# Kernel optimization log

Measured on AMD Instinct MI355X. Metric: run time of the kernel, lower is better.

The kernel has to match this reference:

```python
import jax, jax.numpy as jnp
import numpy as np

DIM = 4096
N_EXPERTS = 64
TOP_K = 2
TOKENS = 16384


def setup_inputs() -> dict:
    key = jax.random.key(0)
    k1, k2 = jax.random.split(key)
    x = jax.random.normal(k1, (TOKENS, DIM), dtype=jnp.float32)
    # nn.Linear weight is [out_features, in_features] = [n_experts, dim]
    w_gate = jax.random.normal(k2, (N_EXPERTS, DIM), dtype=jnp.float32) * (1.0 / np.sqrt(DIM))
    return {"x": x, "w_gate": w_gate}


def reference(x, w_gate):
    # logits: [tokens, n_experts]
    logits = jnp.einsum("td,ed->te", x, w_gate)
    gates = jax.nn.softmax(logits, axis=-1)
    topk_vals, topk_idx = jax.lax.top_k(gates, TOP_K)
    return (gates, topk_vals, topk_idx)
```

## Files before the change

kernel.cpp:

```cpp
#include <hip/hip_runtime.h>
#include <stdint.h>

typedef float f32x4 __attribute__((ext_vector_type(4)));
typedef _Float16 f16;
typedef _Float16 f16x8 __attribute__((ext_vector_type(8)));

#define TOKENS 16384
#define DIM    4096
#define NEXP   64
#define BM     32
#define KC     64
#define NCHUNK (DIM/KC)
#define GSZ    (TOKENS*NEXP)
#define VSZ    (TOKENS*2)
#define BUFSZ  24576
#define LSTR   68

__device__ __forceinline__ void split8(f32x4 a, f32x4 b, f16x8& h, f16x8& l) {
#pragma unroll
    for (int i = 0; i < 4; ++i) {
        float v = a[i]; f16 hi = (f16)v;
        h[i] = hi; l[i] = (f16)(v - (float)hi);
    }
#pragma unroll
    for (int i = 0; i < 4; ++i) {
        float v = b[i]; f16 hi = (f16)v;
        h[4+i] = hi; l[4+i] = (f16)(v - (float)hi);
    }
}

__global__ __launch_bounds__(256, 2)
void router_kernel(const float* __restrict__ x,
                   const float* __restrict__ w,
                   float* __restrict__ out)
{
    __shared__ unsigned char smem[2*BUFSZ];

    const int tid  = threadIdx.x;
    const int tok0 = blockIdx.x * BM;

    const int xrow = tid >> 3, xks = tid & 7;
    const int we   = tid >> 2, wq  = tid & 3;

    const float* xg = x + (size_t)(tok0 + xrow)*DIM + xks*8;
    const float* wg = w + (size_t)we*DIM + wq*16;

    const int lane = tid & 63;
    const int wv   = tid >> 6;
    const int mt   = wv >> 1;
    const int ntb  = (wv & 1) * 2;
    const int frow = mt*16 + (lane & 15);
    const int fk   = lane >> 4;
    const int swz  = lane & 7;

    f32x4 acc[2] = {{0,0,0,0},{0,0,0,0}};

    f32x4 xr0, xr1, wr0, wr1, wr2, wr3;
    xr0 = ((const f32x4*)xg)[0];  xr1 = ((const f32x4*)xg)[1];
    wr0 = ((const f32x4*)wg)[0];  wr1 = ((const f32x4*)wg)[1];
    wr2 = ((const f32x4*)wg)[2];  wr3 = ((const f32x4*)wg)[3];

    auto cw = [&](unsigned char* base) {
        f16* XH = (f16*)base;
        f16* XL = XH + BM*KC;
        f16* WH = XL + BM*KC;
        f16* WL = WH + NEXP*KC;
        f16x8 h, l;
        split8(xr0, xr1, h, l);
        int s = xks ^ (xrow & 7);
        *(f16x8*)(XH + xrow*KC + s*8) = h;
        *(f16x8*)(XL + xrow*KC + s*8) = l;
        split8(wr0, wr1, h, l);
        s = (wq*2) ^ (we & 7);
        *(f16x8*)(WH + we*KC + s*8) = h;
        *(f16x8*)(WL + we*KC + s*8) = l;
        split8(wr2, wr3, h, l);
        s = (wq*2 + 1) ^ (we & 7);
        *(f16x8*)(WH + we*KC + s*8) = h;
        *(f16x8*)(WL + we*KC + s*8) = l;
    };

    cw(smem);

    for (int kc = 0; kc < NCHUNK; ++kc) {
        if (kc + 1 < NCHUNK) {
            const float* xp = xg + (kc+1)*KC;
            const float* wp = wg + (kc+1)*KC;
            xr0 = ((const f32x4*)xp)[0];  xr1 = ((const f32x4*)xp)[1];
            wr0 = ((const f32x4*)wp)[0];  wr1 = ((const f32x4*)wp)[1];
            wr2 = ((const f32x4*)wp)[2];  wr3 = ((const f32x4*)wp)[3];
        }
        asm volatile("s_waitcnt lgkmcnt(0)" ::: "memory");
        __builtin_amdgcn_s_barrier();

        const unsigned char* base = smem + (size_t)(kc & 1)*BUFSZ;
        const f16* XH = (const f16*)base;
        const f16* XL = XH + BM*KC;
        const f16* WH = XL + BM*KC;
        const f16* WL = WH + NEXP*KC;
#pragma unroll
        for (int ks = 0; ks < 2; ++ks) {
            const int sl = (ks*4 + fk) ^ swz;
            f16x8 ah = *(const f16x8*)(XH + frow*KC + sl*8);
            f16x8 al = *(const f16x8*)(XL + frow*KC + sl*8);
#pragma unroll
            for (int n = 0; n < 2; ++n) {
                const int e = (ntb + n)*16 + (lane & 15);
                f16x8 bh = *(const f16x8*)(WH + e*KC + sl*8);
                f16x8 bl = *(const f16x8*)(WL + e*KC + sl*8);
                acc[n] = __builtin_amdgcn_mfma_f32_16x16x32_f16(ah, bh, acc[n], 0, 0, 0);
                acc[n] = __builtin_amdgcn_mfma_f32_16x16x32_f16(ah, bl, acc[n], 0, 0, 0);
                acc[n] = __builtin_amdgcn_mfma_f32_16x16x32_f16(al, bh, acc[n], 0, 0, 0);
            }
        }
        if (kc + 1 < NCHUNK) cw(smem + (size_t)((kc+1) & 1)*BUFSZ);
    }

    float* lg = (float*)smem;
#pragma unroll
    for (int n = 0; n < 2; ++n) {
        const int e = (ntb + n)*16 + (lane & 15);
#pragma unroll
        for (int i = 0; i < 4; ++i) {
            const int trow = mt*16 + fk*4 + i;
            lg[trow*LSTR + e] = acc[n][i];
        }
    }
    __syncthreads();

    const int st = tid >> 3;
    const int sg = tid & 7;
    const float* rowp = lg + st*LSTR + sg*8;
    float g[8];
#pragma unroll
    for (int j = 0; j < 8; ++j) g[j] = rowp[j];
    float m = g[0];
#pragma unroll
    for (int j = 1; j < 8; ++j) m = fmaxf(m, g[j]);
#pragma unroll
    for (int off = 1; off < 8; off <<= 1) m = fmaxf(m, __shfl_xor(m, off));
    float s = 0.f;
#pragma unroll
    for (int j = 0; j < 8; ++j) { g[j] = expf(g[j] - m); s += g[j]; }
#pragma unroll
    for (int off = 1; off < 8; off <<= 1) s += __shfl_xor(s, off);
    const float inv = 1.0f / s;
#pragma unroll
    for (int j = 0; j < 8; ++j) g[j] *= inv;

    const size_t t = (size_t)tok0 + st;
    f32x4 g0 = {g[0],g[1],g[2],g[3]}, g1 = {g[4],g[5],g[6],g[7]};
    *(f32x4*)(out + t*NEXP + sg*8)     = g0;
    *(f32x4*)(out + t*NEXP + sg*8 + 4) = g1;

    float v1 = g[0]; int i1 = sg*8;
    float v2 = -__builtin_inff(); int i2 = 1 << 30;
#pragma unroll
    for (int j = 1; j < 8; ++j) {
        float lv = g[j]; int li = sg*8 + j;
        bool b1 = (lv > v1) || (lv == v1 && li < i1);
        bool b2 = (lv > v2) || (lv == v2 && li < i2);
        float pv1 = v1; int pi1 = i1;
        v1 = b1 ? lv : v1;  i1 = b1 ? li : i1;
        v2 = b1 ? pv1 : (b2 ? lv : v2);
        i2 = b1 ? pi1 : (b2 ? li : i2);
    }
#pragma unroll
    for (int off = 1; off < 8; off <<= 1) {
        float ov1 = __shfl_xor(v1, off); int oi1 = __shfl_xor(i1, off);
        float ov2 = __shfl_xor(v2, off); int oi2 = __shfl_xor(i2, off);
        bool afirst = (v1 > ov1) || (v1 == ov1 && i1 < oi1);
        float nv1, nv2; int ni1, ni2;
        if (afirst) {
            nv1 = v1; ni1 = i1;
            bool b = (v2 > ov1) || (v2 == ov1 && i2 < oi1);
            nv2 = b ? v2 : ov1; ni2 = b ? i2 : oi1;
        } else {
            nv1 = ov1; ni1 = oi1;
            bool b = (ov2 > v1) || (ov2 == v1 && oi2 < i1);
            nv2 = b ? ov2 : v1; ni2 = b ? oi2 : i1;
        }
        v1 = nv1; i1 = ni1; v2 = nv2; i2 = ni2;
    }
    if (sg == 0) {
        out[GSZ + 2*t]           = v1;
        out[GSZ + 2*t + 1]       = v2;
        out[GSZ + VSZ + 2*t]     = (float)i1;
        out[GSZ + VSZ + 2*t + 1] = (float)i2;
    }
}

extern "C" void kernel_launch(void* const* d_in, const int* in_sizes, int n_in,
                              void* d_out, int out_size, void* d_ws, size_t ws_size,
                              hipStream_t stream) {
    (void)in_sizes; (void)n_in; (void)d_ws; (void)ws_size; (void)out_size;
    const float* x = (const float*)d_in[0];
    const float* w = (const float*)d_in[1];
    float* out     = (float*)d_out;
    dim3 grid(TOKENS / BM);
    dim3 block(256);
    router_kernel<<<grid, block, 0, stream>>>(x, w, out);
}
```

Baseline: 380.8 us.

## Pre-split gate weights into fp16 fragments and split-K across eight waves

A small pre-pass kernel splits the fp32 gate weights into hi/lo fp16 halves, stored in MFMA fragment order in the workspace. The main kernel then reads x and weight fragments straight from global memory into registers, with no LDS staging or per-chunk barriers. Each of the eight waves in a 512-thread block handles a K slice for all 32 tokens and 64 experts, and the partial sums are reduced through shared memory. This removes the redundant per-block weight conversion and the LDS round trip. It costs an extra launch, more accumulator registers, and a cross-wave reduction, and it relies on weight fragments being served from cache.

```diff
diff --git a/kernel.cpp b/kernel.cpp
--- a/kernel.cpp
+++ b/kernel.cpp
@@ -9,12 +9,9 @@
 #define DIM    4096
 #define NEXP   64
 #define BM     32
-#define KC     64
-#define NCHUNK (DIM/KC)
 #define GSZ    (TOKENS*NEXP)
 #define VSZ    (TOKENS*2)
-#define BUFSZ  24576
-#define LSTR   68
+#define WFRAG  262144
 
 __device__ __forceinline__ void split8(f32x4 a, f32x4 b, f16x8& h, f16x8& l) {
 #pragma unroll
@@ -29,135 +26,128 @@
     }
 }
 
-__global__ __launch_bounds__(256, 2)
+__global__ void split_w_kernel(const float* __restrict__ w,
+                               f16* __restrict__ WH, f16* __restrict__ WL) {
+    const int s    = blockIdx.x * 256 + threadIdx.x;
+    const int lane = s & 63;
+    const int nt   = (s >> 6) & 3;
+    const int kk   = s >> 8;
+    const int e    = nt*16 + (lane & 15);
+    const int k8   = kk*32 + (lane >> 4)*8;
+    const f32x4* wp = (const f32x4*)(w + (size_t)e*DIM + k8);
+    f32x4 a = wp[0], b = wp[1];
+    f16x8 h, l;
+    split8(a, b, h, l);
+    *(f16x8*)(WH + (size_t)s*8) = h;
+    *(f16x8*)(WL + (size_t)s*8) = l;
+}
+
+__global__ __launch_bounds__(512, 4)
 void router_kernel(const float* __restrict__ x,
-                   const float* __restrict__ w,
+                   const f16* __restrict__ WH, const f16* __restrict__ WL,
                    float* __restrict__ out)
 {
-    __shared__ unsigned char smem[2*BUFSZ];
+    __shared__ float red[4][BM*NEXP];
 
     const int tid  = threadIdx.x;
-    const int tok0 = blockIdx.x * BM;
-
-    const int xrow = tid >> 3, xks = tid & 7;
-    const int we   = tid >> 2, wq  = tid & 3;
-
-    const float* xg = x + (size_t)(tok0 + xrow)*DIM + xks*8;
-    const float* wg = w + (size_t)we*DIM + wq*16;
-
     const int lane = tid & 63;
     const int wv   = tid >> 6;
-    const int mt   = wv >> 1;
-    const int ntb  = (wv & 1) * 2;
-    const int frow = mt*16 + (lane & 15);
-    const int fk   = lane >> 4;
-    const int swz  = lane & 7;
+    const int tok0 = blockIdx.x * BM;
+    const int l15  = lane & 15;
+    const int lk   = lane >> 4;
 
-    f32x4 acc[2] = {{0,0,0,0},{0,0,0,0}};
+    const float* ax = x + (size_t)(tok0 + l15)*DIM + wv*512 + lk*8;
+    const f16x8* BH = (const f16x8*)WH;
+    const f16x8* BL = (const f16x8*)WL;
+    const int kk0 = wv * 16;
 
-    f32x4 xr0, xr1, wr0, wr1, wr2, wr3;
-    xr0 = ((const f32x4*)xg)[0];  xr1 = ((const f32x4*)xg)[1];
-    wr0 = ((const f32x4*)wg)[0];  wr1 = ((const f32x4*)wg)[1];
-    wr2 = ((const f32x4*)wg)[2];  wr3 = ((const f32x4*)wg)[3];
+    f32x4 acc[2][4];
+#pragma unroll
+    for (int m = 0; m < 2; ++m)
+#pragma unroll
+        for (int n = 0; n < 4; ++n) acc[m][n] = (f32x4){0.f,0.f,0.f,0.f};
 
-    auto cw = [&](unsigned char* base) {
-        f16* XH = (f16*)base;
-        f16* XL = XH + BM*KC;
-        f16* WH = XL + BM*KC;
-        f16* WL = WH + NEXP*KC;
-        f16x8 h, l;
-        split8(xr0, xr1, h, l);
-        int s = xks ^ (xrow & 7);
-        *(f16x8*)(XH + xrow*KC + s*8) = h;
-        *(f16x8*)(XL + xrow*KC + s*8) = l;
-        split8(wr0, wr1, h, l);
-        s = (wq*2) ^ (we & 7);
-        *(f16x8*)(WH + we*KC + s*8) = h;
-        *(f16x8*)(WL + we*KC + s*8) = l;
-        split8(wr2, wr3, h, l);
-        s = (wq*2 + 1) ^ (we & 7);
-        *(f16x8*)(WH + we*KC + s*8) = h;
-        *(f16x8*)(WL + we*KC + s*8) = l;
-    };
-
-    cw(smem);
-
-    for (int kc = 0; kc < NCHUNK; ++kc) {
-        if (kc + 1 < NCHUNK) {
-            const float* xp = xg + (kc+1)*KC;
-            const float* wp = wg + (kc+1)*KC;
-            xr0 = ((const f32x4*)xp)[0];  xr1 = ((const f32x4*)xp)[1];
-            wr0 = ((const f32x4*)wp)[0];  wr1 = ((const f32x4*)wp)[1];
-            wr2 = ((const f32x4*)wp)[2];  wr3 = ((const f32x4*)wp)[3];
+#pragma unroll
+    for (int s = 0; s < 16; ++s) {
+        const float* ap = ax + s*32;
+        f32x4 a00 = *(const f32x4*)(ap);
+        f32x4 a01 = *(const f32x4*)(ap + 4);
+        f32x4 a10 = *(const f32x4*)(ap + (size_t)16*DIM);
+        f32x4 a11 = *(const f32x4*)(ap + (size_t)16*DIM + 4);
+        f16x8 bh[4], bl[4];
+#pragma unroll
+        for (int n = 0; n < 4; ++n) {
+            const int idx = ((kk0 + s)*4 + n)*64 + lane;
+            bh[n] = BH[idx];
+            bl[n] = BL[idx];
         }
-        asm volatile("s_waitcnt lgkmcnt(0)" ::: "memory");
-        __builtin_amdgcn_s_barrier();
-
-        const unsigned char* base = smem + (size_t)(kc & 1)*BUFSZ;
-        const f16* XH = (const f16*)base;
-        const f16* XL = XH + BM*KC;
-        const f16* WH = XL + BM*KC;
-        const f16* WL = WH + NEXP*KC;
+        f16x8 ah0, al0, ah1, al1;
+        split8(a00, a01, ah0, al0);
+        split8(a10, a11, ah1, al1);
 #pragma unroll
-        for (int ks = 0; ks < 2; ++ks) {
-            const int sl = (ks*4 + fk) ^ swz;
-            f16x8 ah = *(const f16x8*)(XH + frow*KC + sl*8);
-            f16x8 al = *(const f16x8*)(XL + frow*KC + sl*8);
-#pragma unroll
-            for (int n = 0; n < 2; ++n) {
-                const int e = (ntb + n)*16 + (lane & 15);
-                f16x8 bh = *(const f16x8*)(WH + e*KC + sl*8);
-                f16x8 bl = *(const f16x8*)(WL + e*KC + sl*8);
-                acc[n] = __builtin_amdgcn_mfma_f32_16x16x32_f16(ah, bh, acc[n], 0, 0, 0);
-                acc[n] = __builtin_amdgcn_mfma_f32_16x16x32_f16(ah, bl, acc[n], 0, 0, 0);
-                acc[n] = __builtin_amdgcn_mfma_f32_16x16x32_f16(al, bh, acc[n], 0, 0, 0);
-            }
+        for (int n = 0; n < 4; ++n) {
+            acc[0][n] = __builtin_amdgcn_mfma_f32_16x16x32_f16(ah0, bh[n], acc[0][n], 0, 0, 0);
+            acc[0][n] = __builtin_amdgcn_mfma_f32_16x16x32_f16(ah0, bl[n], acc[0][n], 0, 0, 0);
+            acc[0][n] = __builtin_amdgcn_mfma_f32_16x16x32_f16(al0, bh[n], acc[0][n], 0, 0, 0);
+            acc[1][n] = __builtin_amdgcn_mfma_f32_16x16x32_f16(ah1, bh[n], acc[1][n], 0, 0, 0);
+            acc[1][n] = __builtin_amdgcn_mfma_f32_16x16x32_f16(ah1, bl[n], acc[1][n], 0, 0, 0);
+            acc[1][n] = __builtin_amdgcn_mfma_f32_16x16x32_f16(al1, bh[n], acc[1][n], 0, 0, 0);
         }
-        if (kc + 1 < NCHUNK) cw(smem + (size_t)((kc+1) & 1)*BUFSZ);
     }
 
-    float* lg = (float*)smem;
+    if (wv < 4) {
 #pragma unroll
-    for (int n = 0; n < 2; ++n) {
-        const int e = (ntb + n)*16 + (lane & 15);
+        for (int m = 0; m < 2; ++m)
 #pragma unroll
-        for (int i = 0; i < 4; ++i) {
-            const int trow = mt*16 + fk*4 + i;
-            lg[trow*LSTR + e] = acc[n][i];
-        }
+            for (int n = 0; n < 4; ++n)
+#pragma unroll
+                for (int i = 0; i < 4; ++i)
+                    red[wv][(m*16 + lk*4 + i)*NEXP + n*16 + l15] = acc[m][n][i];
+    }
+    __syncthreads();
+    if (wv >= 4) {
+#pragma unroll
+        for (int m = 0; m < 2; ++m)
+#pragma unroll
+            for (int n = 0; n < 4; ++n)
+#pragma unroll
+                for (int i = 0; i < 4; ++i)
+                    red[wv-4][(m*16 + lk*4 + i)*NEXP + n*16 + l15] += acc[m][n][i];
     }
     __syncthreads();
 
-    const int st = tid >> 3;
-    const int sg = tid & 7;
-    const float* rowp = lg + st*LSTR + sg*8;
-    float g[8];
+    const int st = tid >> 4;
+    const int sg = tid & 15;
+    const int ei = st*NEXP + sg*4;
+    f32x4 s0 = *(const f32x4*)(&red[0][ei]);
+    f32x4 s1 = *(const f32x4*)(&red[1][ei]);
+    f32x4 s2 = *(const f32x4*)(&red[2][ei]);
+    f32x4 s3 = *(const f32x4*)(&red[3][ei]);
+    f32x4 lt = (s0 + s1) + (s2 + s3);
+    float l[4] = {lt[0], lt[1], lt[2], lt[3]};
+
+    float m = fmaxf(fmaxf(l[0], l[1]), fmaxf(l[2], l[3]));
 #pragma unroll
-    for (int j = 0; j < 8; ++j) g[j] = rowp[j];
-    float m = g[0];
+    for (int off = 1; off < 16; off <<= 1) m = fmaxf(m, __shfl_xor(m, off));
+    float g[4];
+    float ssum = 0.f;
 #pragma unroll
-    for (int j = 1; j < 8; ++j) m = fmaxf(m, g[j]);
+    for (int j = 0; j < 4; ++j) { g[j] = expf(l[j] - m); ssum += g[j]; }
 #pragma unroll
-    for (int off = 1; off < 8; off <<= 1) m = fmaxf(m, __shfl_xor(m, off));
-    float s = 0.f;
+    for (int off = 1; off < 16; off <<= 1) ssum += __shfl_xor(ssum, off);
+    const float inv = 1.0f / ssum;
 #pragma unroll
-    for (int j = 0; j < 8; ++j) { g[j] = expf(g[j] - m); s += g[j]; }
-#pragma unroll
-    for (int off = 1; off < 8; off <<= 1) s += __shfl_xor(s, off);
-    const float inv = 1.0f / s;
-#pragma unroll
-    for (int j = 0; j < 8; ++j) g[j] *= inv;
+    for (int j = 0; j < 4; ++j) g[j] *= inv;
 
     const size_t t = (size_t)tok0 + st;
-    f32x4 g0 = {g[0],g[1],g[2],g[3]}, g1 = {g[4],g[5],g[6],g[7]};
-    *(f32x4*)(out + t*NEXP + sg*8)     = g0;
-    *(f32x4*)(out + t*NEXP + sg*8 + 4) = g1;
+    f32x4 gv = {g[0], g[1], g[2], g[3]};
+    *(f32x4*)(out + t*NEXP + sg*4) = gv;
 
-    float v1 = g[0]; int i1 = sg*8;
+    float v1 = g[0]; int i1 = sg*4;
     float v2 = -__builtin_inff(); int i2 = 1 << 30;
 #pragma unroll
-    for (int j = 1; j < 8; ++j) {
-        float lv = g[j]; int li = sg*8 + j;
+    for (int j = 1; j < 4; ++j) {
+        float lv = g[j]; int li = sg*4 + j;
         bool b1 = (lv > v1) || (lv == v1 && li < i1);
         bool b2 = (lv > v2) || (lv == v2 && li < i2);
         float pv1 = v1; int pi1 = i1;
@@ -166,7 +156,7 @@
         i2 = b1 ? pi1 : (b2 ? li : i2);
     }
 #pragma unroll
-    for (int off = 1; off < 8; off <<= 1) {
+    for (int off = 1; off < 16; off <<= 1) {
         float ov1 = __shfl_xor(v1, off); int oi1 = __shfl_xor(i1, off);
         float ov2 = __shfl_xor(v2, off); int oi2 = __shfl_xor(i2, off);
         bool afirst = (v1 > ov1) || (v1 == ov1 && i1 < oi1);
@@ -193,11 +183,13 @@
 extern "C" void kernel_launch(void* const* d_in, const int* in_sizes, int n_in,
                               void* d_out, int out_size, void* d_ws, size_t ws_size,
                               hipStream_t stream) {
-    (void)in_sizes; (void)n_in; (void)d_ws; (void)ws_size; (void)out_size;
+    (void)in_sizes; (void)n_in; (void)ws_size; (void)out_size;
     const float* x = (const float*)d_in[0];
     const float* w = (const float*)d_in[1];
     float* out     = (float*)d_out;
-    dim3 grid(TOKENS / BM);
-    dim3 block(256);
-    router_kernel<<<grid, block, 0, stream>>>(x, w, out);
+    f16* WH = (f16*)d_ws;
+    f16* WL = WH + WFRAG;
+
+    split_w_kernel<<<128, 256, 0, stream>>>(w, WH, WL);
+    router_kernel<<<TOKENS/BM, 512, 0, stream>>>(x, WH, WL, out);
 }
```

Measured after the change: 374.5 us. Within noise of the previous version (-1.7%).
